# Kernel tuning notes

Hardware: AMD Instinct MI355X
Metric: run time of the kernel (lower is better)

## Reference

```python
import jax, jax.numpy as jnp
import numpy as np

N, E = 50000, 800000
D_IN, D_HID, D_OUT = 128, 64, 32
NEG_SLOPE = 0.2


def _gat_layer(h_in, src, dst, W, a_s, a_d, b):
    # h_in: [N, din], W: [din, dout]
    h = h_in @ W                                   # [N, dout]
    alpha_src = h @ a_s                            # [N]
    alpha_dst = h @ a_d                            # [N]
    e = jax.nn.leaky_relu(alpha_src[src] + alpha_dst[dst], NEG_SLOPE)  # [E']
    # segment softmax over incoming edges of each dst node
    m = jax.ops.segment_max(e, dst, num_segments=N)
    ex = jnp.exp(e - m[dst])
    s = jax.ops.segment_sum(ex, dst, num_segments=N)
    w = ex / s[dst]                                # [E']
    out = jax.ops.segment_sum(h[src] * w[:, None], dst, num_segments=N)
    return out + b


def setup_inputs() -> dict:
    key = jax.random.key(0)
    ks = jax.random.split(key, 16)
    x = jax.random.normal(ks[0], (N, D_IN), dtype=jnp.float32)
    edge_index = jax.random.randint(ks[1], (2, E), 0, N, dtype=jnp.int64)
    dims = [(D_IN, D_HID), (D_HID, D_HID), (D_HID, D_OUT)]
    inp = {"x": x, "edge_index": edge_index}
    for i, (din, dout) in enumerate(dims):
        sc = 1.0 / np.sqrt(din)
        inp[f"W{i}"] = jax.random.normal(ks[2 + 4 * i], (din, dout), dtype=jnp.float32) * sc
        inp[f"as{i}"] = jax.random.normal(ks[3 + 4 * i], (dout,), dtype=jnp.float32) * 0.1
        inp[f"ad{i}"] = jax.random.normal(ks[4 + 4 * i], (dout,), dtype=jnp.float32) * 0.1
        inp[f"b{i}"] = jnp.zeros((dout,), dtype=jnp.float32)
    return inp


def reference(x, edge_index, W0, as0, ad0, b0, W1, as1, ad1, b1, W2, as2, ad2, b2):
    # add self loops (PyG GATConv default)
    loop = jnp.arange(N, dtype=edge_index.dtype)
    src = jnp.concatenate([edge_index[0], loop])
    dst = jnp.concatenate([edge_index[1], loop])
    h = jax.nn.relu(_gat_layer(x, src, dst, W0, as0, ad0, b0))
    h = jax.nn.relu(_gat_layer(h, src, dst, W1, as1, ad1, b1))
    h = jnp.tanh(_gat_layer(h, src, dst, W2, as2, ad2, b2))
    return h
```

## Files before the change

### kernel.cpp

```cpp
#include <hip/hip_runtime.h>
#include <hip/hip_fp16.h>
#include <math.h>

#define N_NODES 50000
#define E_EDGES 800000
#define ETOT    (E_EDGES + N_NODES)

#define BUCK_SHIFT 9
#define BUCK_SZ   (1 << BUCK_SHIFT)
#define NBUCK ((N_NODES + BUCK_SZ - 1) >> BUCK_SHIFT)
#define BS_EPT 16
#define BS_THREADS 256
#define BS_EPB (BS_THREADS * BS_EPT)
#define BS_NBLK ((ETOT + BS_EPB - 1) / BS_EPB)

#define CAP_SHIFT 14
#define CAP (1 << CAP_SHIFT)

#define GEMM0_GRID ((N_NODES + 63) / 64)
#define PACK_GRID (GEMM0_GRID + BS_NBLK)

__global__ __launch_bounds__(256)
void gemm0_binscatter_kernel(const float* __restrict__ X,
                             const float* __restrict__ W,
                             const float* __restrict__ a_s,
                             const float* __restrict__ a_d,
                             __half* __restrict__ H16,
                             float* __restrict__ asrc,
                             float* __restrict__ adst,
                             const int* __restrict__ ei,
                             int* __restrict__ cur,
                             unsigned int* __restrict__ tmp)
{
    __shared__ float smem[128 * 64];
    const int t = threadIdx.x;

    if (blockIdx.x < GEMM0_GRID) {
        constexpr int DIN = 128, DOUT = 64, COLG = 16;
        float* Wl = smem;
        for (int i = t; i < DIN * DOUT / 4; i += 256)
            ((float4*)Wl)[i] = ((const float4*)W)[i];
        __syncthreads();

        const int row0b = blockIdx.x * 64;
        const int tx = t % COLG;
        const int ty = t / COLG;
        const int r0 = ty * 4;
        const int c0 = tx * 4;

        const float* Xr[4];
#pragma unroll
        for (int i = 0; i < 4; ++i) {
            int gr = row0b + r0 + i;
            Xr[i] = X + (size_t)min(gr, N_NODES - 1) * DIN;
        }

        float acc[4][4] = {};
#pragma unroll 4
        for (int kk = 0; kk < DIN; kk += 4) {
            float a[4][4], w[4][4];
#pragma unroll
            for (int i = 0; i < 4; ++i)
                *(float4*)a[i] = *(const float4*)&Xr[i][kk];
#pragma unroll
            for (int j = 0; j < 4; ++j)
                *(float4*)w[j] = *(const float4*)&Wl[(kk + j) * DOUT + c0];
#pragma unroll
            for (int i = 0; i < 4; ++i)
#pragma unroll
                for (int j = 0; j < 4; ++j)
                    acc[i][j] = fmaf(a[i][0], w[0][j],
                                fmaf(a[i][1], w[1][j],
                                fmaf(a[i][2], w[2][j],
                                fmaf(a[i][3], w[3][j], acc[i][j]))));
        }

        float as4[4], ad4[4];
        *(float4*)as4 = *(const float4*)&a_s[c0];
        *(float4*)ad4 = *(const float4*)&a_d[c0];

#pragma unroll
        for (int i = 0; i < 4; ++i) {
            const int gr = row0b + r0 + i;
            float ps = acc[i][0] * as4[0] + acc[i][1] * as4[1] +
                       acc[i][2] * as4[2] + acc[i][3] * as4[3];
            float pd = acc[i][0] * ad4[0] + acc[i][1] * ad4[1] +
                       acc[i][2] * ad4[2] + acc[i][3] * ad4[3];
#pragma unroll
            for (int off = COLG / 2; off >= 1; off >>= 1) {
                ps += __shfl_xor(ps, off, 64);
                pd += __shfl_xor(pd, off, 64);
            }
            if (gr < N_NODES) {
                __half2 p01 = __floats2half2_rn(acc[i][0], acc[i][1]);
                __half2 p23 = __floats2half2_rn(acc[i][2], acc[i][3]);
                uint2 pk;
                pk.x = *(unsigned int*)&p01;
                pk.y = *(unsigned int*)&p23;
                *(uint2*)&H16[gr * DOUT + c0] = pk;
                if (tx == 0) { asrc[gr] = ps; adst[gr] = pd; }
            }
        }
    } else {
        int* lcnt  = (int*)smem;
        int* lbase = lcnt + 128;

        for (int i = t; i < NBUCK; i += 256) lcnt[i] = 0;
        __syncthreads();

        const int e0 = (blockIdx.x - GEMM0_GRID) * BS_EPB;
        unsigned int pk[BS_EPT];
        int rk[BS_EPT];
        int bk[BS_EPT];
#pragma unroll
        for (int k = 0; k < BS_EPT; ++k) {
            const int eid = e0 + k * BS_THREADS + t;
            bk[k] = -1;
            if (eid < ETOT) {
                int src, dst;
                if (eid < E_EDGES) { src = ei[eid]; dst = ei[E_EDGES + eid]; }
                else               { src = dst = eid - E_EDGES; }
                bk[k] = dst >> BUCK_SHIFT;
                pk[k] = ((unsigned int)dst << 16) | (unsigned int)src;
                rk[k] = atomicAdd(&lcnt[bk[k]], 1);
            }
        }
        __syncthreads();
        for (int i = t; i < NBUCK; i += 256)
            if (lcnt[i] > 0)
                lbase[i] = (i << CAP_SHIFT) + atomicAdd(&cur[i], lcnt[i]);
        __syncthreads();
#pragma unroll
        for (int k = 0; k < BS_EPT; ++k)
            if (bk[k] >= 0) tmp[lbase[bk[k]] + rk[k]] = pk[k];
    }
}

__global__ __launch_bounds__(BUCK_SZ)
void bucket_sort_kernel(const unsigned int* __restrict__ tmp,
                        const int* __restrict__ cur,
                        unsigned int* __restrict__ csr_pk,
                        int* __restrict__ offs)
{
    __shared__ int lcnt[BUCK_SZ];
    __shared__ int loff[BUCK_SZ];
    __shared__ int lcur[BUCK_SZ];
    __shared__ int sbase;
    const int bk = blockIdx.x;
    const int t  = threadIdx.x;

    {
        const int v = (t < NBUCK) ? cur[t] : 0;
        lcnt[t] = v;
        __syncthreads();
        for (int off = 1; off < 128; off <<= 1) {
            int u = (t >= off && t < 128) ? lcnt[t - off] : 0;
            __syncthreads();
            if (t < 128) lcnt[t] += u;
            __syncthreads();
        }
        if (t == bk) sbase = lcnt[t] - v;
    }
    __syncthreads();
    const int base  = sbase;
    const int tbase = bk << CAP_SHIFT;
    const int cnt   = cur[bk];

    lcnt[t] = 0;
    __syncthreads();
    for (int i = t; i < cnt; i += BUCK_SZ)
        atomicAdd(&lcnt[(tmp[tbase + i] >> 16) & (BUCK_SZ - 1)], 1);
    __syncthreads();

    const int v = lcnt[t];
    loff[t] = v;
    __syncthreads();
    for (int off = 1; off < BUCK_SZ; off <<= 1) {
        int u = (t >= off) ? loff[t - off] : 0;
        __syncthreads();
        loff[t] += u;
        __syncthreads();
    }
    const int excl = loff[t] - v;

    const int g = (bk << BUCK_SHIFT) + t;
    if (g <= N_NODES) offs[g] = base + excl;

    lcur[t] = excl;
    __syncthreads();
    for (int i = t; i < cnt; i += BUCK_SZ) {
        const unsigned int pk = tmp[tbase + i];
        const int l = (pk >> 16) & (BUCK_SZ - 1);
        const int pos = atomicAdd(&lcur[l], 1);
        csr_pk[base + pos] = pk;
    }
}

template<int DIN, int DOUT>
__global__ __launch_bounds__(256)
void gemm_alpha_kernel(const float* __restrict__ X, const float* __restrict__ W,
                       const float* __restrict__ a_s, const float* __restrict__ a_d,
                       __half* __restrict__ H16, float* __restrict__ asrc,
                       float* __restrict__ adst)
{
    constexpr int COLG = DOUT / 4;
    constexpr int ROWG = 256 / COLG;
    constexpr int BM   = ROWG * 4;

    __shared__ float Wl[DIN * DOUT];

    const int tid = threadIdx.x;
    const int row0b = blockIdx.x * BM;

    for (int i = tid; i < DIN * DOUT / 4; i += 256)
        ((float4*)Wl)[i] = ((const float4*)W)[i];
    __syncthreads();

    const int tx = tid % COLG;
    const int ty = tid / COLG;
    const int r0 = ty * 4;
    const int c0 = tx * 4;

    const float* Xr[4];
#pragma unroll
    for (int i = 0; i < 4; ++i) {
        int gr = row0b + r0 + i;
        Xr[i] = X + (size_t)min(gr, N_NODES - 1) * DIN;
    }

    float acc[4][4] = {};
#pragma unroll 4
    for (int kk = 0; kk < DIN; kk += 4) {
        float a[4][4], w[4][4];
#pragma unroll
        for (int i = 0; i < 4; ++i)
            *(float4*)a[i] = *(const float4*)&Xr[i][kk];
#pragma unroll
        for (int j = 0; j < 4; ++j)
            *(float4*)w[j] = *(const float4*)&Wl[(kk + j) * DOUT + c0];
#pragma unroll
        for (int i = 0; i < 4; ++i)
#pragma unroll
            for (int j = 0; j < 4; ++j)
                acc[i][j] = fmaf(a[i][0], w[0][j],
                            fmaf(a[i][1], w[1][j],
                            fmaf(a[i][2], w[2][j],
                            fmaf(a[i][3], w[3][j], acc[i][j]))));
    }

    float as4[4], ad4[4];
    *(float4*)as4 = *(const float4*)&a_s[c0];
    *(float4*)ad4 = *(const float4*)&a_d[c0];

#pragma unroll
    for (int i = 0; i < 4; ++i) {
        const int gr = row0b + r0 + i;
        float ps = acc[i][0] * as4[0] + acc[i][1] * as4[1] +
                   acc[i][2] * as4[2] + acc[i][3] * as4[3];
        float pd = acc[i][0] * ad4[0] + acc[i][1] * ad4[1] +
                   acc[i][2] * ad4[2] + acc[i][3] * ad4[3];
#pragma unroll
        for (int off = COLG / 2; off >= 1; off >>= 1) {
            ps += __shfl_xor(ps, off, 64);
            pd += __shfl_xor(pd, off, 64);
        }
        if (gr < N_NODES) {
            __half2 p01 = __floats2half2_rn(acc[i][0], acc[i][1]);
            __half2 p23 = __floats2half2_rn(acc[i][2], acc[i][3]);
            uint2 pk;
            pk.x = *(unsigned int*)&p01;
            pk.y = *(unsigned int*)&p23;
            *(uint2*)&H16[gr * DOUT + c0] = pk;
            if (tx == 0) { asrc[gr] = ps; adst[gr] = pd; }
        }
    }
}

template<int DOUT, int ACT>
__global__ __launch_bounds__(256)
void node_agg_kernel(const int* __restrict__ offs,
                     const unsigned int* __restrict__ csr_pk,
                     const float* __restrict__ asrc,
                     const float* __restrict__ adst,
                     const __half* __restrict__ H16,
                     const float* __restrict__ b,
                     float* __restrict__ out)
{
    constexpr int FL    = DOUT / 8;
    constexpr int SLOTS = 64 / FL;
    const int wv   = threadIdx.x >> 6;
    const int lane = threadIdx.x & 63;
    const int fl   = lane % FL;
    const int slot = lane / FL;
    const int node = blockIdx.x * 4 + wv;
    if (node >= N_NODES) return;

    const int beg = offs[node];
    const int end = offs[node + 1];
    const float adn = adst[node];
    const __half* __restrict__ Hf = H16 + fl * 8;

    float s = 0.f;
    float acc[8] = {};

    int eid = beg + slot;
    bool valid = (eid < end);
    unsigned int pk = valid ? csr_pk[eid] : 0u;

    for (int cb = beg; cb < end; cb += SLOTS) {
        const int nid = cb + SLOTS + slot;
        const bool nvalid = (nid < end);
        const unsigned int npk = nvalid ? csr_pk[nid] : 0u;

        float p = 0.f;
        uint4 h = make_uint4(0u, 0u, 0u, 0u);
        if (valid) {
            const unsigned int src = pk & 0xffffu;
            float v = asrc[src] + adn;
            v = fmaxf(v, 0.2f * v);
            p = __expf(fminf(v, 80.f));
            h = *(const uint4*)(Hf + src * DOUT);
        }
        const float2 f0 = __half22float2(*(const __half2*)&h.x);
        const float2 f1 = __half22float2(*(const __half2*)&h.y);
        const float2 f2 = __half22float2(*(const __half2*)&h.z);
        const float2 f3 = __half22float2(*(const __half2*)&h.w);
        s += p;
        acc[0] = fmaf(p, f0.x, acc[0]);
        acc[1] = fmaf(p, f0.y, acc[1]);
        acc[2] = fmaf(p, f1.x, acc[2]);
        acc[3] = fmaf(p, f1.y, acc[3]);
        acc[4] = fmaf(p, f2.x, acc[4]);
        acc[5] = fmaf(p, f2.y, acc[5]);
        acc[6] = fmaf(p, f3.x, acc[6]);
        acc[7] = fmaf(p, f3.y, acc[7]);
        valid = nvalid;
        pk = npk;
    }

#pragma unroll
    for (int off = FL; off < 64; off <<= 1) {
        s += __shfl_xor(s, off, 64);
#pragma unroll
        for (int j = 0; j < 8; ++j)
            acc[j] += __shfl_xor(acc[j], off, 64);
    }

    if (slot == 0) {
        const float inv = 1.f / s;
        float o[8];
#pragma unroll
        for (int j = 0; j < 8; ++j) {
            float v = acc[j] * inv + b[fl * 8 + j];
            o[j] = (ACT == 0) ? fmaxf(v, 0.f) : tanhf(v);
        }
        *(float4*)&out[node * DOUT + fl * 8]     = *(float4*)&o[0];
        *(float4*)&out[node * DOUT + fl * 8 + 4] = *(float4*)&o[4];
    }
}


extern "C" void kernel_launch(void* const* d_in, const int* in_sizes, int n_in,
                              void* d_out, int out_size, void* d_ws, size_t ws_size,
                              hipStream_t stream)
{
    const float* x  = (const float*)d_in[0];
    const int*   ei = (const int*)d_in[1];
    const float* W0 = (const float*)d_in[2];
    const float* as0= (const float*)d_in[3];
    const float* ad0= (const float*)d_in[4];
    const float* b0 = (const float*)d_in[5];
    const float* W1 = (const float*)d_in[6];
    const float* as1= (const float*)d_in[7];
    const float* ad1= (const float*)d_in[8];
    const float* b1 = (const float*)d_in[9];
    const float* W2 = (const float*)d_in[10];
    const float* as2= (const float*)d_in[11];
    const float* ad2= (const float*)d_in[12];
    const float* b2 = (const float*)d_in[13];
    float* out = (float*)d_out;

    char* wsb = (char*)d_ws;
    auto take = [&](size_t bytes) {
        char* p = wsb;
        wsb += (bytes + 255) & ~size_t(255);
        return p;
    };
    __half* h16    = (__half*)take(sizeof(__half) * N_NODES * 64);
    float* buf_act = (float*)take(sizeof(float) * N_NODES * 64);
    float* asrc    = (float*)take(sizeof(float) * N_NODES);
    float* adst    = (float*)take(sizeof(float) * N_NODES);
    int*   offs    = (int*)take(sizeof(int) * (N_NODES + 1));
    int*   cur     = (int*)take(sizeof(int) * NBUCK);
    unsigned int* tmp    = (unsigned int*)take(sizeof(unsigned int) * NBUCK * CAP);
    unsigned int* csr_pk = (unsigned int*)take(sizeof(unsigned int) * ETOT);

    hipMemsetAsync(cur, 0, sizeof(int) * NBUCK, stream);

    gemm0_binscatter_kernel<<<PACK_GRID, 256, 0, stream>>>(
        x, W0, as0, ad0, h16, asrc, adst, ei, cur, tmp);

    bucket_sort_kernel<<<NBUCK, BUCK_SZ, 0, stream>>>(tmp, cur, csr_pk, offs);

    const int agg_grid = (N_NODES + 3) / 4;
    node_agg_kernel<64, 0><<<agg_grid, 256, 0, stream>>>(
        offs, csr_pk, asrc, adst, h16, b0, buf_act);

    gemm_alpha_kernel<64, 64><<<GEMM0_GRID, 256, 0, stream>>>(
        buf_act, W1, as1, ad1, h16, asrc, adst);
    node_agg_kernel<64, 0><<<agg_grid, 256, 0, stream>>>(
        offs, csr_pk, asrc, adst, h16, b1, buf_act);

    gemm_alpha_kernel<64, 32><<<(N_NODES + 127) / 128, 256, 0, stream>>>(
        buf_act, W2, as2, ad2, h16, asrc, adst);
    node_agg_kernel<32, 1><<<agg_grid, 256, 0, stream>>>(
        offs, csr_pk, asrc, adst, h16, b2, out);
}
```

Baseline: 163.7 us.

## Fuse aggregation with next layer's GEMM and attention projections

Merges each layer's edge aggregation kernel with the following layer's dense transform and alpha computation. Each wave aggregates one node into shared memory and then computes that node's next-layer features, so the fp32 activation buffer no longer makes a round trip through global memory and two launches are removed. Ping-pong half-precision buffers avoid read/write hazards. In exchange, every block of only four nodes reloads the full weight matrix into shared memory, and the per-node GEMM is a scalar dot product that reuses little data.

```diff
diff --git a/kernel.cpp b/kernel.cpp
--- a/kernel.cpp
+++ b/kernel.cpp
@@ -19,6 +19,7 @@
 
 #define GEMM0_GRID ((N_NODES + 63) / 64)
 #define PACK_GRID (GEMM0_GRID + BS_NBLK)
+#define AGG_GRID ((N_NODES + 3) / 4)
 
 __global__ __launch_bounds__(256)
 void gemm0_binscatter_kernel(const float* __restrict__ X,
@@ -196,83 +197,124 @@
     }
 }
 
-template<int DIN, int DOUT>
+template<int DOUT_NEXT>
 __global__ __launch_bounds__(256)
-void gemm_alpha_kernel(const float* __restrict__ X, const float* __restrict__ W,
-                       const float* __restrict__ a_s, const float* __restrict__ a_d,
-                       __half* __restrict__ H16, float* __restrict__ asrc,
-                       float* __restrict__ adst)
+void agg_gemm_kernel(const int* __restrict__ offs,
+                     const unsigned int* __restrict__ csr_pk,
+                     const float* __restrict__ asrc_p,
+                     const float* __restrict__ adst_p,
+                     const __half* __restrict__ H16_p,
+                     const float* __restrict__ b_p,
+                     const float* __restrict__ W,
+                     const float* __restrict__ a_s,
+                     const float* __restrict__ a_d,
+                     __half* __restrict__ H16_n,
+                     float* __restrict__ asrc_n,
+                     float* __restrict__ adst_n)
 {
-    constexpr int COLG = DOUT / 4;
-    constexpr int ROWG = 256 / COLG;
-    constexpr int BM   = ROWG * 4;
-
-    __shared__ float Wl[DIN * DOUT];
-
-    const int tid = threadIdx.x;
-    const int row0b = blockIdx.x * BM;
-
-    for (int i = tid; i < DIN * DOUT / 4; i += 256)
+    constexpr int DIN = 64;
+    constexpr int FL = 8, SLOTS = 8;
+    __shared__ float Wl[DIN * DOUT_NEXT];
+    __shared__ float act[4][DIN];
+
+    const int t = threadIdx.x;
+    const int wv   = t >> 6;
+    const int lane = t & 63;
+    const int fl   = lane % FL;
+    const int slot = lane / FL;
+    const int node = blockIdx.x * 4 + wv;
+
+    for (int i = t; i < DIN * DOUT_NEXT / 4; i += 256)
         ((float4*)Wl)[i] = ((const float4*)W)[i];
-    __syncthreads();
-
-    const int tx = tid % COLG;
-    const int ty = tid / COLG;
-    const int r0 = ty * 4;
-    const int c0 = tx * 4;
-
-    const float* Xr[4];
-#pragma unroll
-    for (int i = 0; i < 4; ++i) {
-        int gr = row0b + r0 + i;
-        Xr[i] = X + (size_t)min(gr, N_NODES - 1) * DIN;
-    }
-
-    float acc[4][4] = {};
-#pragma unroll 4
-    for (int kk = 0; kk < DIN; kk += 4) {
-        float a[4][4], w[4][4];
-#pragma unroll
-        for (int i = 0; i < 4; ++i)
-            *(float4*)a[i] = *(const float4*)&Xr[i][kk];
-#pragma unroll
-        for (int j = 0; j < 4; ++j)
-            *(float4*)w[j] = *(const float4*)&Wl[(kk + j) * DOUT + c0];
-#pragma unroll
-        for (int i = 0; i < 4; ++i)
-#pragma unroll
-            for (int j = 0; j < 4; ++j)
-                acc[i][j] = fmaf(a[i][0], w[0][j],
-                            fmaf(a[i][1], w[1][j],
-                            fmaf(a[i][2], w[2][j],
-                            fmaf(a[i][3], w[3][j], acc[i][j]))));
-    }
-
-    float as4[4], ad4[4];
-    *(float4*)as4 = *(const float4*)&a_s[c0];
-    *(float4*)ad4 = *(const float4*)&a_d[c0];
-
-#pragma unroll
-    for (int i = 0; i < 4; ++i) {
-        const int gr = row0b + r0 + i;
-        float ps = acc[i][0] * as4[0] + acc[i][1] * as4[1] +
-                   acc[i][2] * as4[2] + acc[i][3] * as4[3];
-        float pd = acc[i][0] * ad4[0] + acc[i][1] * ad4[1] +
-                   acc[i][2] * ad4[2] + acc[i][3] * ad4[3];
-#pragma unroll
-        for (int off = COLG / 2; off >= 1; off >>= 1) {
-            ps += __shfl_xor(ps, off, 64);
-            pd += __shfl_xor(pd, off, 64);
-        }
-        if (gr < N_NODES) {
-            __half2 p01 = __floats2half2_rn(acc[i][0], acc[i][1]);
-            __half2 p23 = __floats2half2_rn(acc[i][2], acc[i][3]);
-            uint2 pk;
-            pk.x = *(unsigned int*)&p01;
-            pk.y = *(unsigned int*)&p23;
-            *(uint2*)&H16[gr * DOUT + c0] = pk;
-            if (tx == 0) { asrc[gr] = ps; adst[gr] = pd; }
-        }
+
+    int beg = 0, end = 0;
+    float adn = 0.f;
+    if (node < N_NODES) {
+        beg = offs[node];
+        end = offs[node + 1];
+        adn = adst_p[node];
+    }
+    const __half* __restrict__ Hf = H16_p + fl * 8;
+
+    float s = 0.f;
+    float acc[8] = {};
+
+    int eid = beg + slot;
+    bool valid = (eid < end);
+    unsigned int pk = valid ? csr_pk[eid] : 0u;
+
+    for (int cb = beg; cb < end; cb += SLOTS) {
+        const int nid = cb + SLOTS + slot;
+        const bool nvalid = (nid < end);
+        const unsigned int npk = nvalid ? csr_pk[nid] : 0u;
+
+        float p = 0.f;
+        uint4 h = make_uint4(0u, 0u, 0u, 0u);
+        if (valid) {
+            const unsigned int src = pk & 0xffffu;
+            float v = asrc_p[src] + adn;
+            v = fmaxf(v, 0.2f * v);
+            p = __expf(fminf(v, 80.f));
+            h = *(const uint4*)(Hf + src * DIN);
+        }
+        const float2 f0 = __half22float2(*(const __half2*)&h.x);
+        const float2 f1 = __half22float2(*(const __half2*)&h.y);
+        const float2 f2 = __half22float2(*(const __half2*)&h.z);
+        const float2 f3 = __half22float2(*(const __half2*)&h.w);
+        s += p;
+        acc[0] = fmaf(p, f0.x, acc[0]);
+        acc[1] = fmaf(p, f0.y, acc[1]);
+        acc[2] = fmaf(p, f1.x, acc[2]);
+        acc[3] = fmaf(p, f1.y, acc[3]);
+        acc[4] = fmaf(p, f2.x, acc[4]);
+        acc[5] = fmaf(p, f2.y, acc[5]);
+        acc[6] = fmaf(p, f3.x, acc[6]);
+        acc[7] = fmaf(p, f3.y, acc[7]);
+        valid = nvalid;
+        pk = npk;
+    }
+
+#pragma unroll
+    for (int off = FL; off < 64; off <<= 1) {
+        s += __shfl_xor(s, off, 64);
+#pragma unroll
+        for (int j = 0; j < 8; ++j)
+            acc[j] += __shfl_xor(acc[j], off, 64);
+    }
+
+    if (slot == 0) {
+        float o[8];
+        if (node < N_NODES) {
+            const float inv = 1.f / s;
+#pragma unroll
+            for (int j = 0; j < 8; ++j)
+                o[j] = fmaxf(acc[j] * inv + b_p[fl * 8 + j], 0.f);
+        } else {
+#pragma unroll
+            for (int j = 0; j < 8; ++j) o[j] = 0.f;
+        }
+#pragma unroll
+        for (int j = 0; j < 8; ++j) act[wv][fl * 8 + j] = o[j];
+    }
+    __syncthreads();
+
+    const int c = lane;
+    float h = 0.f;
+    if (c < DOUT_NEXT) {
+#pragma unroll 8
+        for (int k = 0; k < DIN; ++k)
+            h = fmaf(act[wv][k], Wl[k * DOUT_NEXT + c], h);
+    }
+    float ps = (c < DOUT_NEXT) ? h * a_s[c] : 0.f;
+    float pd = (c < DOUT_NEXT) ? h * a_d[c] : 0.f;
+#pragma unroll
+    for (int off = 32; off >= 1; off >>= 1) {
+        ps += __shfl_xor(ps, off, 64);
+        pd += __shfl_xor(pd, off, 64);
+    }
+    if (node < N_NODES) {
+        if (c < DOUT_NEXT) H16_n[node * DOUT_NEXT + c] = __float2half(h);
+        if (lane == 0) { asrc_n[node] = ps; adst_n[node] = pd; }
     }
 }
 
@@ -386,10 +428,12 @@
         wsb += (bytes + 255) & ~size_t(255);
         return p;
     };
-    __half* h16    = (__half*)take(sizeof(__half) * N_NODES * 64);
-    float* buf_act = (float*)take(sizeof(float) * N_NODES * 64);
-    float* asrc    = (float*)take(sizeof(float) * N_NODES);
-    float* adst    = (float*)take(sizeof(float) * N_NODES);
+    __half* h16a   = (__half*)take(sizeof(__half) * N_NODES * 64);
+    __half* h16b   = (__half*)take(sizeof(__half) * N_NODES * 64);
+    float* asrc_a  = (float*)take(sizeof(float) * N_NODES);
+    float* adst_a  = (float*)take(sizeof(float) * N_NODES);
+    float* asrc_b  = (float*)take(sizeof(float) * N_NODES);
+    float* adst_b  = (float*)take(sizeof(float) * N_NODES);
     int*   offs    = (int*)take(sizeof(int) * (N_NODES + 1));
     int*   cur     = (int*)take(sizeof(int) * NBUCK);
     unsigned int* tmp    = (unsigned int*)take(sizeof(unsigned int) * NBUCK * CAP);
@@ -398,21 +442,18 @@
     hipMemsetAsync(cur, 0, sizeof(int) * NBUCK, stream);
 
     gemm0_binscatter_kernel<<<PACK_GRID, 256, 0, stream>>>(
-        x, W0, as0, ad0, h16, asrc, adst, ei, cur, tmp);
+        x, W0, as0, ad0, h16a, asrc_a, adst_a, ei, cur, tmp);
 
     bucket_sort_kernel<<<NBUCK, BUCK_SZ, 0, stream>>>(tmp, cur, csr_pk, offs);
 
-    const int agg_grid = (N_NODES + 3) / 4;
-    node_agg_kernel<64, 0><<<agg_grid, 256, 0, stream>>>(
-        offs, csr_pk, asrc, adst, h16, b0, buf_act);
-
-    gemm_alpha_kernel<64, 64><<<GEMM0_GRID, 256, 0, stream>>>(
-        buf_act, W1, as1, ad1, h16, asrc, adst);
-    node_agg_kernel<64, 0><<<agg_grid, 256, 0, stream>>>(
-        offs, csr_pk, asrc, adst, h16, b1, buf_act);
-
-    gemm_alpha_kernel<64, 32><<<(N_NODES + 127) / 128, 256, 0, stream>>>(
-        buf_act, W2, as2, ad2, h16, asrc, adst);
-    node_agg_kernel<32, 1><<<agg_grid, 256, 0, stream>>>(
-        offs, csr_pk, asrc, adst, h16, b2, out);
+    agg_gemm_kernel<64><<<AGG_GRID, 256, 0, stream>>>(
+        offs, csr_pk, asrc_a, adst_a, h16a, b0,
+        W1, as1, ad1, h16b, asrc_b, adst_b);
+
+    agg_gemm_kernel<32><<<AGG_GRID, 256, 0, stream>>>(
+        offs, csr_pk, asrc_b, adst_b, h16b, b1,
+        W2, as2, ad2, h16a, asrc_a, adst_a);
+
+    node_agg_kernel<32, 1><<<AGG_GRID, 256, 0, stream>>>(
+        offs, csr_pk, asrc_a, adst_a, h16a, b2, out);
 }
```

After: 178.0 us. +8.8%, slower.
